# Kernel tuning notes

Hardware: AMD Instinct MI355X
Metric: run time of the kernel (lower is better)

## Reference

```python
import jax, jax.numpy as jnp
import numpy as np

N_NODES = 20000
N_EDGES = 640000
N_GRAPHS = 64
HID = 256
NF = 128
NG = 100   # edge_channels / num_gaussians
NBLK = 6
CUTOFF = 10.0
LOG2 = float(np.log(2.0))


def setup_inputs() -> dict:
    key = jax.random.key(0)
    ks = jax.random.split(key, 24)
    inp = {}
    inp['atom_types'] = jax.random.randint(ks[0], (N_NODES,), 0, 100)
    inp['edge_index'] = jax.random.randint(ks[1], (2, N_EDGES), 0, N_NODES)
    inp['edge_length'] = jax.random.uniform(ks[2], (N_EDGES, 1), jnp.float32) * CUTOFF
    inp['batch_seg'] = jnp.sort(jax.random.randint(ks[3], (N_NODES,), 0, N_GRAPHS))
    s = 0.05
    # embedding table (Embedding(100, hidden); init small so max_norm=10 renorm is inactive)
    inp['atom_emb'] = jax.random.normal(ks[4], (100, HID), jnp.float32) * 0.5
    # per-interaction-block params, stacked on a leading block axis; weights stored [in, out]
    inp['W1s'] = jax.random.normal(ks[5], (NBLK, NG, NF), jnp.float32) * s      # filter MLP lin1
    inp['b1s'] = jnp.zeros((NBLK, NF), jnp.float32)
    inp['W2s'] = jax.random.normal(ks[6], (NBLK, NF, NF), jnp.float32) * s      # filter MLP lin2
    inp['b2s'] = jnp.zeros((NBLK, NF), jnp.float32)
    inp['lin1Ws'] = jax.random.normal(ks[7], (NBLK, HID, NF), jnp.float32) * s  # CFConv.lin1 (no bias)
    inp['lin2Ws'] = jax.random.normal(ks[8], (NBLK, NF, HID), jnp.float32) * s  # CFConv.lin2
    inp['lin2bs'] = jnp.zeros((NBLK, HID), jnp.float32)
    inp['linWs'] = jax.random.normal(ks[9], (NBLK, HID, HID), jnp.float32) * s  # InteractionBlock.lin
    inp['linbs'] = jnp.zeros((NBLK, HID), jnp.float32)
    # final MLP: Linear(256,256) -> act -> Linear(256,256)
    inp['fW1'] = jax.random.normal(ks[10], (HID, HID), jnp.float32) * s
    inp['fb1'] = jnp.zeros((HID,), jnp.float32)
    inp['fW2'] = jax.random.normal(ks[11], (HID, HID), jnp.float32) * s
    inp['fb2'] = jnp.zeros((HID,), jnp.float32)
    return inp


def _ssp(x):
    # ShiftedSoftplus: softplus(x) - log(2)
    return jax.nn.softplus(x) - LOG2


def reference(atom_emb, W1s, b1s, W2s, b2s, lin1Ws, lin2Ws, lin2bs, linWs, linbs,
              fW1, fb1, fW2, fb2, edge_length, atom_types, edge_index, batch_seg):
    n = atom_types.shape[0]
    h = atom_emb[atom_types]                                     # [N, H]
    # Gaussian smearing edge encoder: exp(-0.5/dg^2 * (d - mu_k)^2)
    offsets = jnp.linspace(0.0, CUTOFF, NG)
    coeff = -0.5 / (offsets[1] - offsets[0]) ** 2
    edge_attr = jnp.exp(coeff * (edge_length - offsets[None, :]) ** 2)  # [E, NG]
    # smooth=False cutoff gate
    C = (edge_length <= CUTOFF).astype(h.dtype)                  # [E, 1]
    src, dst = edge_index[0], edge_index[1]
    for i in range(NBLK):
        W = _ssp(edge_attr @ W1s[i] + b1s[i]) @ W2s[i] + b2s[i]  # [E, F]
        W = W * C
        xf = h @ lin1Ws[i]                                       # [N, F]
        msg = xf[src] * W                                        # gather + filter: [E, F]
        agg = jax.ops.segment_sum(msg, dst, num_segments=n)      # scatter-add: [N, F]
        hc = _ssp(agg @ lin2Ws[i] + lin2bs[i])
        hc = hc @ linWs[i] + linbs[i]
        h = h + hc                                               # residual
    pooled = jax.ops.segment_max(h, batch_seg, num_segments=N_GRAPHS)  # global_max_pool
    out = jax.nn.relu(pooled @ fW1 + fb1) @ fW2 + fb2
    return out
```

## Files before the change

kernel.cpp:

```cpp
#include <hip/hip_runtime.h>
#include <math.h>

#define HID 256
#define NF 128
#define NGAUSS 100
#define NBLK 6
#define NGRAPH 64
#define CUTOFF_F 10.0f
#define T_TAB 2048

typedef __attribute__((ext_vector_type(8))) short bf16x8;
typedef __attribute__((ext_vector_type(4))) float f32x4;

__device__ __forceinline__ float ssp(float x) {
    return fmaxf(x, 0.0f) + log1pf(expf(-fabsf(x))) - 0.69314718056f;
}
__device__ __forceinline__ short f2bf(float f) {
    unsigned u = __float_as_uint(f);
    u = u + 0x7fffu + ((u >> 16) & 1u);
    return (short)(u >> 16);
}
__device__ __forceinline__ float bf2f(unsigned s) {
    return __uint_as_float(s << 16);
}
__device__ __forceinline__ unsigned enc_f(float f) {
    unsigned b = __float_as_uint(f);
    return (b & 0x80000000u) ? ~b : (b | 0x80000000u);
}
__device__ __forceinline__ float dec_f(unsigned u) {
    unsigned b = (u & 0x80000000u) ? (u & 0x7FFFFFFFu) : ~u;
    return __uint_as_float(b);
}

__global__ __launch_bounds__(256) void prep_weights(
        const float* __restrict__ W1s,   short* __restrict__ W1Tb,
        const float* __restrict__ W2s,   short* __restrict__ W2Tb,
        const float* __restrict__ lin1Ws, short* __restrict__ lin1T,
        const float* __restrict__ lin2Ws, short* __restrict__ W2T,
        const float* __restrict__ linWs,  short* __restrict__ W3T)
{
    const float* in; short* out; int Ks, Kp, C;
    switch (blockIdx.z) {
        case 0: in = W1s;    out = W1Tb;  Ks = NGAUSS; Kp = NF;  C = NF;  break;
        case 1: in = W2s;    out = W2Tb;  Ks = NF;     Kp = NF;  C = NF;  break;
        case 2: in = lin1Ws; out = lin1T; Ks = HID;    Kp = HID; C = NF;  break;
        case 3: in = lin2Ws; out = W2T;   Ks = NF;     Kp = NF;  C = HID; break;
        default: in = linWs; out = W3T;   Ks = HID;    Kp = HID; C = HID; break;
    }
    int i = blockIdx.y;
    int idx = blockIdx.x * 256 + threadIdx.x;
    if (idx >= Kp * C) return;
    int k = idx / C, c = idx % C;
    out[((size_t)i * C + c) * Kp + k] =
        (k < Ks) ? f2bf(in[((size_t)i * Ks + k) * C + c]) : (short)0;
}

__global__ __launch_bounds__(256) void build_table_mfma(
        const short* __restrict__ W1T, const float* __restrict__ b1s,
        const short* __restrict__ W2T, const float* __restrict__ b2s,
        short* __restrict__ Wtab)
{
    __shared__ short Gs[32 * NF];
    __shared__ short Hs[32 * NF];
    char* gb = (char*)Gs;
    char* hb = (char*)Hs;
    const int i = blockIdx.y;
    const int r0 = blockIdx.x * 32;
    const int wv = threadIdx.x >> 6, lane = threadIdx.x & 63;
    const int lrow = lane & 15, lgrp = lane >> 4;

    const float delta = CUTOFF_F / 99.0f;
    const float coeff = -0.5f / (delta * delta);
    for (int idx = threadIdx.x; idx < 32 * NF; idx += 256) {
        int row = idx >> 7, k = idx & 127;
        float d = (float)(r0 + row) * (CUTOFF_F / (float)(T_TAB - 1));
        float x = d - (float)k * delta;
        float v = (k < NGAUSS) ? expf(coeff * x * x) : 0.0f;
        int byte = idx * 2;
        byte ^= (row & 7) << 4;
        *(short*)(gb + byte) = f2bf(v);
    }
    __syncthreads();

    f32x4 zero = {0.0f, 0.0f, 0.0f, 0.0f};
    f32x4 c1[2][2] = {{zero, zero}, {zero, zero}};
    for (int s = 0; s < 4; ++s) {
        bf16x8 a[2], b[2];
        #pragma unroll
        for (int m = 0; m < 2; ++m) {
            int row = m * 16 + lrow;
            int byte = (row * NF + s * 32 + lgrp * 8) * 2;
            byte ^= (row & 7) << 4;
            a[m] = *(const bf16x8*)(gb + byte);
        }
        #pragma unroll
        for (int n = 0; n < 2; ++n) {
            int col = wv * 32 + n * 16 + lrow;
            b[n] = *(const bf16x8*)(W1T + ((size_t)i * NF + col) * NF + s * 32 + lgrp * 8);
        }
        #pragma unroll
        for (int m = 0; m < 2; ++m)
            #pragma unroll
            for (int n = 0; n < 2; ++n)
                c1[m][n] = __builtin_amdgcn_mfma_f32_16x16x32_bf16(a[m], b[n], c1[m][n], 0, 0, 0);
    }
    #pragma unroll
    for (int m = 0; m < 2; ++m)
        #pragma unroll
        for (int n = 0; n < 2; ++n) {
            int col = wv * 32 + n * 16 + lrow;
            float bb = b1s[i * NF + col];
            #pragma unroll
            for (int j = 0; j < 4; ++j) {
                int row = m * 16 + lgrp * 4 + j;
                int byte = (row * NF + col) * 2;
                byte ^= (row & 7) << 4;
                *(short*)(hb + byte) = f2bf(ssp(c1[m][n][j] + bb));
            }
        }
    __syncthreads();

    f32x4 c2[2][2] = {{zero, zero}, {zero, zero}};
    for (int s = 0; s < 4; ++s) {
        bf16x8 a[2], b[2];
        #pragma unroll
        for (int m = 0; m < 2; ++m) {
            int row = m * 16 + lrow;
            int byte = (row * NF + s * 32 + lgrp * 8) * 2;
            byte ^= (row & 7) << 4;
            a[m] = *(const bf16x8*)(hb + byte);
        }
        #pragma unroll
        for (int n = 0; n < 2; ++n) {
            int col = wv * 32 + n * 16 + lrow;
            b[n] = *(const bf16x8*)(W2T + ((size_t)i * NF + col) * NF + s * 32 + lgrp * 8);
        }
        #pragma unroll
        for (int m = 0; m < 2; ++m)
            #pragma unroll
            for (int n = 0; n < 2; ++n)
                c2[m][n] = __builtin_amdgcn_mfma_f32_16x16x32_bf16(a[m], b[n], c2[m][n], 0, 0, 0);
    }
    #pragma unroll
    for (int m = 0; m < 2; ++m)
        #pragma unroll
        for (int n = 0; n < 2; ++n) {
            int col = wv * 32 + n * 16 + lrow;
            float bb = b2s[i * NF + col];
            #pragma unroll
            for (int j = 0; j < 4; ++j) {
                int t = r0 + m * 16 + lgrp * 4 + j;
                Wtab[((size_t)i * T_TAB + t) * NF + col] = f2bf(c2[m][n][j] + bb);
            }
        }
}

__global__ __launch_bounds__(256) void pack_wtab(
        const short* __restrict__ Wtab, uint2* __restrict__ WtabP)
{
    size_t idx = (size_t)blockIdx.x * 256 + threadIdx.x;
    if (idx >= (size_t)NBLK * (T_TAB + 1) * 64) return;
    int l = (int)(idx & 63);
    int t = (int)((idx >> 6) % (T_TAB + 1));
    int i = (int)(idx / ((size_t)64 * (T_TAB + 1)));
    if (t == T_TAB) { WtabP[idx] = make_uint2(0u, 0u); return; }
    int t1 = (t + 1 < T_TAB) ? t + 1 : t;
    unsigned a = *((const unsigned*)(Wtab + ((size_t)i * T_TAB + t)  * NF) + l);
    unsigned b = *((const unsigned*)(Wtab + ((size_t)i * T_TAB + t1) * NF) + l);
    WtabP[idx] = make_uint2(a, b);
}

__global__ __launch_bounds__(256) void embed_k(
        const float* __restrict__ emb, const int* __restrict__ types,
        float* __restrict__ h, int N)
{
    int gid = blockIdx.x * 256 + threadIdx.x;
    if (gid >= N * HID) return;
    int n = gid >> 8, c = gid & (HID - 1);
    h[gid] = emb[(size_t)types[n] * HID + c];
}

__global__ __launch_bounds__(256) void hist_k(
        const int* __restrict__ dst, int* __restrict__ hist, int E)
{
    int e = blockIdx.x * 256 + threadIdx.x;
    if (e < E) atomicAdd(&hist[dst[e]], 1);
}

__global__ __launch_bounds__(1024) void scan_k(
        const int* __restrict__ in, int* __restrict__ out, int n)
{
    __shared__ int wsum[16];
    __shared__ int carry_s;
    const int tid = threadIdx.x, lane = tid & 63, w = tid >> 6;
    if (tid == 0) carry_s = 0;
    __syncthreads();
    for (int base = 0; base < n; base += 1024) {
        int i = base + tid;
        int v = (i < n) ? in[i] : 0;
        int s = v;
        #pragma unroll
        for (int d = 1; d < 64; d <<= 1) {
            int t = __shfl_up(s, d);
            if (lane >= d) s += t;
        }
        if (lane == 63) wsum[w] = s;
        __syncthreads();
        if (w == 0 && lane < 16) {
            int ws = wsum[lane];
            #pragma unroll
            for (int d = 1; d < 16; d <<= 1) {
                int t = __shfl_up(ws, d);
                if (lane >= d) ws += t;
            }
            wsum[lane] = ws;
        }
        __syncthreads();
        int carry = carry_s;
        if (i < n) out[i] = carry + (w ? wsum[w - 1] : 0) + s - v;
        __syncthreads();
        if (tid == 1023) carry_s = carry + wsum[15];
        __syncthreads();
    }
    if (threadIdx.x == 0) out[n] = carry_s;
}

__global__ __launch_bounds__(256) void scatter_k(
        const int* __restrict__ src, const int* __restrict__ dst,
        const float* __restrict__ elen, const int* __restrict__ off,
        int* __restrict__ cursor, unsigned long long* __restrict__ csr_pk, int E)
{
    int e = blockIdx.x * 256 + threadIdx.x;
    if (e >= E) return;
    int t = dst[e];
    int pos = off[t] + atomicAdd(&cursor[t], 1);
    float d = elen[e];
    float u = d * ((float)(T_TAB - 1) / CUTOFF_F);
    u = fminf(fmaxf(u, 0.0f), (float)(T_TAB - 1) - 1e-3f);
    u = (d <= CUTOFF_F) ? u : (float)T_TAB;
    csr_pk[pos] = ((unsigned long long)__float_as_uint(u) << 32) | (unsigned)src[e];
}

__global__ __launch_bounds__(256) void sort_k(
        const int* __restrict__ off, unsigned long long* __restrict__ csr_pk, int N)
{
    const int node = (blockIdx.x * 256 + threadIdx.x) >> 6;
    const int lane = threadIdx.x & 63;
    if (node >= N) return;
    const int beg = off[node], end = off[node + 1];
    const int deg = end - beg;
    if (deg <= 1) return;
    if (deg <= 128) {
        const unsigned long long PAD = ~0ull;
        unsigned long long v0 = (lane < deg) ? csr_pk[beg + lane] : PAD;
        unsigned long long v1 = (64 + lane < deg) ? csr_pk[beg + 64 + lane] : PAD;
        if (deg > 64) {
            for (int size = 2; size <= 128; size <<= 1)
                for (int stride = size >> 1; stride > 0; stride >>= 1) {
                    if (stride == 64) {
                        unsigned long long lo = v0 < v1 ? v0 : v1;
                        unsigned long long hi = v0 < v1 ? v1 : v0;
                        v0 = lo; v1 = hi;
                    } else {
                        unsigned long long p0 = __shfl_xor(v0, stride);
                        unsigned long long p1 = __shfl_xor(v1, stride);
                        bool up = (lane & stride) != 0;
                        bool d0 = ((lane & size) == 0);
                        bool d1 = (((lane + 64) & size) == 0);
                        v0 = (up ^ d0) ? (v0 < p0 ? v0 : p0) : (v0 > p0 ? v0 : p0);
                        v1 = (up ^ d1) ? (v1 < p1 ? v1 : p1) : (v1 > p1 ? v1 : p1);
                    }
                }
            if (lane < deg) csr_pk[beg + lane] = v0;
            if (64 + lane < deg) csr_pk[beg + 64 + lane] = v1;
        } else {
            for (int size = 2; size <= 64; size <<= 1)
                for (int stride = size >> 1; stride > 0; stride >>= 1) {
                    unsigned long long p0 = __shfl_xor(v0, stride);
                    bool up = (lane & stride) != 0;
                    bool d0 = ((lane & size) == 0);
                    v0 = (up ^ d0) ? (v0 < p0 ? v0 : p0) : (v0 > p0 ? v0 : p0);
                }
            if (lane < deg) csr_pk[beg + lane] = v0;
        }
    } else if (lane == 0) {
        for (int a = beg + 1; a < end; ++a) {
            unsigned long long key = csr_pk[a];
            int b = a - 1;
            while (b >= beg && csr_pk[b] > key) { csr_pk[b + 1] = csr_pk[b]; --b; }
            csr_pk[b + 1] = key;
        }
    }
}


__global__ __launch_bounds__(256) void lin1_k(
        const float* __restrict__ h, const short* __restrict__ lin1T,
        short* __restrict__ xf, int N)
{
    const int wv = threadIdx.x >> 6, lane = threadIdx.x & 63;
    const int lrow = lane & 15, lgrp = lane >> 4;
    const int wrow = wv >> 1, wcol = wv & 1;
    const int r0 = blockIdx.x * 64 + wrow * 32;

    f32x4 zero = {0.0f, 0.0f, 0.0f, 0.0f};
    f32x4 c[2][4] = {{zero, zero, zero, zero}, {zero, zero, zero, zero}};

    for (int s = 0; s < 8; ++s) {
        bf16x8 a[2], b[4];
        #pragma unroll
        for (int m = 0; m < 2; ++m) {
            int row = r0 + m * 16 + lrow;
            if (row >= N) row = N - 1;
            const float* hp = h + (size_t)row * HID + s * 32 + lgrp * 8;
            float4 p0 = *(const float4*)hp;
            float4 p1 = *(const float4*)(hp + 4);
            bf16x8 t;
            t[0] = f2bf(p0.x); t[1] = f2bf(p0.y); t[2] = f2bf(p0.z); t[3] = f2bf(p0.w);
            t[4] = f2bf(p1.x); t[5] = f2bf(p1.y); t[6] = f2bf(p1.z); t[7] = f2bf(p1.w);
            a[m] = t;
        }
        #pragma unroll
        for (int n = 0; n < 4; ++n) {
            int col = wcol * 64 + n * 16 + lrow;
            b[n] = *(const bf16x8*)(lin1T + (size_t)col * HID + s * 32 + lgrp * 8);
        }
        #pragma unroll
        for (int m = 0; m < 2; ++m)
            #pragma unroll
            for (int n = 0; n < 4; ++n)
                c[m][n] = __builtin_amdgcn_mfma_f32_16x16x32_bf16(a[m], b[n], c[m][n], 0, 0, 0);
    }
    #pragma unroll
    for (int m = 0; m < 2; ++m)
        #pragma unroll
        for (int n = 0; n < 4; ++n) {
            int col = wcol * 64 + n * 16 + lrow;
            #pragma unroll
            for (int j = 0; j < 4; ++j) {
                int row = r0 + m * 16 + lgrp * 4 + j;
                if (row < N) xf[(size_t)row * NF + col] = f2bf(c[m][n][j]);
            }
        }
}

__global__ __launch_bounds__(256) void agg_k(
        const short* __restrict__ xf, const uint2* __restrict__ wt,
        const int* __restrict__ off, const unsigned long long* __restrict__ csr_pk,
        short* __restrict__ agg, int N)
{
    const int node = (blockIdx.x * 256 + threadIdx.x) >> 6;
    const int lane = threadIdx.x & 63;
    if (node >= N) return;
    const int beg = __builtin_amdgcn_readfirstlane(off[node]);
    const int end = __builtin_amdgcn_readfirstlane(off[node + 1]);
    float a0 = 0.0f, a1 = 0.0f;

    int k = beg;
    for (; k + 16 <= end; k += 16) {
        unsigned long long pk[16];
        #pragma unroll
        for (int q = 0; q < 16; ++q) pk[q] = csr_pk[k + q];
        uint2 wp[16];
        unsigned xv[16];
        float fr[16];
        #pragma unroll
        for (int q = 0; q < 16; ++q) {
            int s = (int)(unsigned)pk[q];
            float uf = __uint_as_float((unsigned)(pk[q] >> 32));
            int i0 = (int)uf;
            fr[q] = uf - (float)i0;
            wp[q] = wt[(size_t)i0 * 64 + lane];
            xv[q] = *(const unsigned*)(xf + (size_t)s * NF + 2 * lane);
        }
        #pragma unroll
        for (int q = 0; q < 16; ++q) {
            float w0a = bf2f(wp[q].x & 0xffffu), w0b = bf2f(wp[q].x >> 16);
            float w1a = bf2f(wp[q].y & 0xffffu), w1b = bf2f(wp[q].y >> 16);
            float xa  = bf2f(xv[q] & 0xffffu), xb  = bf2f(xv[q] >> 16);
            a0 = fmaf(xa, fmaf(fr[q], w1a - w0a, w0a), a0);
            a1 = fmaf(xb, fmaf(fr[q], w1b - w0b, w0b), a1);
        }
    }
    for (; k + 8 <= end; k += 8) {
        unsigned long long pk[8];
        #pragma unroll
        for (int q = 0; q < 8; ++q) pk[q] = csr_pk[k + q];
        uint2 wp[8];
        unsigned xv[8];
        float fr[8];
        #pragma unroll
        for (int q = 0; q < 8; ++q) {
            int s = (int)(unsigned)pk[q];
            float uf = __uint_as_float((unsigned)(pk[q] >> 32));
            int i0 = (int)uf;
            fr[q] = uf - (float)i0;
            wp[q] = wt[(size_t)i0 * 64 + lane];
            xv[q] = *(const unsigned*)(xf + (size_t)s * NF + 2 * lane);
        }
        #pragma unroll
        for (int q = 0; q < 8; ++q) {
            float w0a = bf2f(wp[q].x & 0xffffu), w0b = bf2f(wp[q].x >> 16);
            float w1a = bf2f(wp[q].y & 0xffffu), w1b = bf2f(wp[q].y >> 16);
            float xa  = bf2f(xv[q] & 0xffffu), xb  = bf2f(xv[q] >> 16);
            a0 = fmaf(xa, fmaf(fr[q], w1a - w0a, w0a), a0);
            a1 = fmaf(xb, fmaf(fr[q], w1b - w0b, w0b), a1);
        }
    }
    if (k < end) {
        const int rem = end - k;
        unsigned long long pk[8];
        #pragma unroll
        for (int q = 0; q < 8; ++q) {
            int kk = k + q < end ? k + q : end - 1;
            pk[q] = csr_pk[kk];
        }
        uint2 wp[8];
        unsigned xv[8];
        float fr[8];
        #pragma unroll
        for (int q = 0; q < 8; ++q) {
            int s = (int)(unsigned)pk[q];
            float uf = __uint_as_float((unsigned)(pk[q] >> 32));
            int i0 = (int)uf;
            fr[q] = uf - (float)i0;
            wp[q] = wt[(size_t)i0 * 64 + lane];
            xv[q] = *(const unsigned*)(xf + (size_t)s * NF + 2 * lane);
        }
        #pragma unroll
        for (int q = 0; q < 8; ++q) {
            float g = (q < rem) ? 1.0f : 0.0f;
            float w0a = bf2f(wp[q].x & 0xffffu), w0b = bf2f(wp[q].x >> 16);
            float w1a = bf2f(wp[q].y & 0xffffu), w1b = bf2f(wp[q].y >> 16);
            float xa  = bf2f(xv[q] & 0xffffu), xb  = bf2f(xv[q] >> 16);
            a0 = fmaf(xa * g, fmaf(fr[q], w1a - w0a, w0a), a0);
            a1 = fmaf(xb * g, fmaf(fr[q], w1b - w0b, w0b), a1);
        }
    }
    unsigned pack = (unsigned)(unsigned short)f2bf(a0)
                  | ((unsigned)(unsigned short)f2bf(a1) << 16);
    *(unsigned*)(agg + (size_t)node * NF + 2 * lane) = pack;
}

__global__ __launch_bounds__(512) void update_k(
        const short* __restrict__ aggb, const short* __restrict__ W2T,
        const float* __restrict__ b2, const short* __restrict__ W3T,
        const float* __restrict__ b3, float* __restrict__ h,
        const short* __restrict__ lin1Tn, short* __restrict__ xf_out, int N)
{
    __shared__ short tmp[32 * HID];
    __shared__ float ftmp[32][HID + 4];
    char* tb = (char*)tmp;
    const int wv = threadIdx.x >> 6, lane = threadIdx.x & 63;
    const int lrow = lane & 15, lgrp = lane >> 4;
    const int r0 = blockIdx.x * 32;

    f32x4 zero = {0.0f, 0.0f, 0.0f, 0.0f};
    f32x4 c1[2][2] = {{zero, zero}, {zero, zero}};

    for (int s = 0; s < 4; ++s) {
        bf16x8 a[2], b[2];
        #pragma unroll
        for (int m = 0; m < 2; ++m) {
            int row = r0 + m * 16 + lrow;
            if (row >= N) row = N - 1;
            a[m] = *(const bf16x8*)(aggb + (size_t)row * NF + s * 32 + lgrp * 8);
        }
        #pragma unroll
        for (int n = 0; n < 2; ++n) {
            int col = wv * 32 + n * 16 + lrow;
            b[n] = *(const bf16x8*)(W2T + (size_t)col * NF + s * 32 + lgrp * 8);
        }
        #pragma unroll
        for (int m = 0; m < 2; ++m)
            #pragma unroll
            for (int n = 0; n < 2; ++n)
                c1[m][n] = __builtin_amdgcn_mfma_f32_16x16x32_bf16(a[m], b[n], c1[m][n], 0, 0, 0);
    }
    #pragma unroll
    for (int m = 0; m < 2; ++m)
        #pragma unroll
        for (int n = 0; n < 2; ++n) {
            int col = wv * 32 + n * 16 + lrow;
            float bb = b2[col];
            #pragma unroll
            for (int j = 0; j < 4; ++j) {
                int row = m * 16 + lgrp * 4 + j;
                int byte = (row * HID + col) * 2;
                byte ^= (row & 7) << 4;
                *(short*)(tb + byte) = f2bf(ssp(c1[m][n][j] + bb));
            }
        }
    __syncthreads();

    f32x4 c2[2][2] = {{zero, zero}, {zero, zero}};
    for (int s = 0; s < 8; ++s) {
        bf16x8 a[2], b[2];
        #pragma unroll
        for (int m = 0; m < 2; ++m) {
            int row = m * 16 + lrow;
            int byte = (row * HID + s * 32 + lgrp * 8) * 2;
            byte ^= (row & 7) << 4;
            a[m] = *(const bf16x8*)(tb + byte);
        }
        #pragma unroll
        for (int n = 0; n < 2; ++n) {
            int col = wv * 32 + n * 16 + lrow;
            b[n] = *(const bf16x8*)(W3T + (size_t)col * HID + s * 32 + lgrp * 8);
        }
        #pragma unroll
        for (int m = 0; m < 2; ++m)
            #pragma unroll
            for (int n = 0; n < 2; ++n)
                c2[m][n] = __builtin_amdgcn_mfma_f32_16x16x32_bf16(a[m], b[n], c2[m][n], 0, 0, 0);
    }

    #pragma unroll
    for (int m = 0; m < 2; ++m)
        #pragma unroll
        for (int n = 0; n < 2; ++n) {
            int col = wv * 32 + n * 16 + lrow;
            float bb = b3[col];
            #pragma unroll
            for (int j = 0; j < 4; ++j)
                ftmp[m * 16 + lgrp * 4 + j][col] = c2[m][n][j] + bb;
        }
    __syncthreads();

    {
        const int r  = threadIdx.x >> 4;
        const int c0 = (threadIdx.x & 15) * 4;
        const int row = r0 + r;
        const bool valid = row < N;
        float* hp = h + (size_t)row * HID;
        #pragma unroll
        for (int k = 0; k < 4; ++k) {
            int col = c0 + k * 64;
            float4 hv = valid ? *(const float4*)(hp + col)
                              : make_float4(0.f, 0.f, 0.f, 0.f);
            float4 f = *(const float4*)&ftmp[r][col];
            hv.x += f.x; hv.y += f.y; hv.z += f.z; hv.w += f.w;
            if (valid) *(float4*)(hp + col) = hv;
            short4 s4;
            s4.x = f2bf(hv.x); s4.y = f2bf(hv.y); s4.z = f2bf(hv.z); s4.w = f2bf(hv.w);
            int byte = (r * HID + col) * 2;
            byte ^= (r & 7) << 4;
            *(short4*)(tb + byte) = s4;
        }
    }
    if (xf_out == nullptr) return;
    __syncthreads();

    f32x4 c3[2] = {zero, zero};
    for (int s = 0; s < 8; ++s) {
        bf16x8 a[2], b;
        #pragma unroll
        for (int m = 0; m < 2; ++m) {
            int row = m * 16 + lrow;
            int byte = (row * HID + s * 32 + lgrp * 8) * 2;
            byte ^= (row & 7) << 4;
            a[m] = *(const bf16x8*)(tb + byte);
        }
        {
            int col = wv * 16 + lrow;
            b = *(const bf16x8*)(lin1Tn + (size_t)col * HID + s * 32 + lgrp * 8);
        }
        #pragma unroll
        for (int m = 0; m < 2; ++m)
            c3[m] = __builtin_amdgcn_mfma_f32_16x16x32_bf16(a[m], b, c3[m], 0, 0, 0);
    }
    #pragma unroll
    for (int m = 0; m < 2; ++m) {
        int col = wv * 16 + lrow;
        #pragma unroll
        for (int j = 0; j < 4; ++j) {
            int row = r0 + m * 16 + lgrp * 4 + j;
            if (row < N) xf_out[(size_t)row * NF + col] = f2bf(c3[m][j]);
        }
    }
}

__global__ __launch_bounds__(256) void pool_init(unsigned* __restrict__ pe)
{
    int i = blockIdx.x * 256 + threadIdx.x;
    if (i < NGRAPH * HID) pe[i] = enc_f(-INFINITY);
}

__global__ __launch_bounds__(256) void pool_max2(
        const float* __restrict__ h, const int* __restrict__ seg,
        unsigned* __restrict__ pe, int N)
{
    const int c = threadIdx.x;
    const int base = blockIdx.x * 64;
    if (base >= N) return;
    int cur = seg[base];
    float m = -INFINITY;
    for (int r = 0; r < 64; ++r) {
        int row = base + r;
        if (row >= N) break;
        int s = seg[row];
        if (s != cur) {
            atomicMax(&pe[(size_t)cur * HID + c], enc_f(m));
            m = -INFINITY;
            cur = s;
        }
        m = fmaxf(m, h[(size_t)row * HID + c]);
    }
    atomicMax(&pe[(size_t)cur * HID + c], enc_f(m));
}

__global__ __launch_bounds__(1024) void final_mlp(
        const unsigned* __restrict__ pe,
        const float* __restrict__ fW1, const float* __restrict__ fb1,
        const float* __restrict__ fW2, const float* __restrict__ fb2,
        float* __restrict__ out)
{
    __shared__ float p[HID];
    __shared__ float part[4][HID];
    __shared__ float p2[HID];
    const int g = blockIdx.x;
    const int c = threadIdx.x & 255;
    const int kq = threadIdx.x >> 8;
    if (threadIdx.x < HID) p[threadIdx.x] = dec_f(pe[(size_t)g * HID + threadIdx.x]);
    __syncthreads();
    float a = 0.0f;
    #pragma unroll 8
    for (int k = kq * 64; k < kq * 64 + 64; ++k)
        a = fmaf(p[k], fW1[(size_t)k * HID + c], a);
    part[kq][c] = a;
    __syncthreads();
    if (kq == 0) {
        float s = part[0][c] + part[1][c] + part[2][c] + part[3][c] + fb1[c];
        p2[c] = fmaxf(s, 0.0f);
    }
    __syncthreads();
    float o = 0.0f;
    #pragma unroll 8
    for (int k = kq * 64; k < kq * 64 + 64; ++k)
        o = fmaf(p2[k], fW2[(size_t)k * HID + c], o);
    part[kq][c] = o;
    __syncthreads();
    if (kq == 0)
        out[(size_t)g * HID + c] = part[0][c] + part[1][c] + part[2][c] + part[3][c] + fb2[c];
}

extern "C" void kernel_launch(void* const* d_in, const int* in_sizes, int n_in,
                              void* d_out, int out_size, void* d_ws, size_t ws_size,
                              hipStream_t stream)
{
    const int*   atom_types = (const int*)  d_in[0];
    const int*   edge_index = (const int*)  d_in[1];
    const float* edge_len   = (const float*)d_in[2];
    const int*   batch_seg  = (const int*)  d_in[3];
    const float* atom_emb   = (const float*)d_in[4];
    const float* W1s    = (const float*)d_in[5];
    const float* b1s    = (const float*)d_in[6];
    const float* W2s    = (const float*)d_in[7];
    const float* b2s    = (const float*)d_in[8];
    const float* lin1Ws = (const float*)d_in[9];
    const float* lin2Ws = (const float*)d_in[10];
    const float* lin2bs = (const float*)d_in[11];
    const float* linWs  = (const float*)d_in[12];
    const float* linbs  = (const float*)d_in[13];
    const float* fW1    = (const float*)d_in[14];
    const float* fb1    = (const float*)d_in[15];
    const float* fW2    = (const float*)d_in[16];
    const float* fb2    = (const float*)d_in[17];

    const int N = in_sizes[0];
    const int E = in_sizes[1] / 2;
    const int* src = edge_index;
    const int* dst = edge_index + E;

    char* ws = (char*)d_ws;
    float* h     = (float*)ws;  ws += (size_t)N * HID * sizeof(float);
    short* xf    = (short*)ws;  ws += (size_t)N * NF * sizeof(short);
    short* aggb  = (short*)ws;  ws += (size_t)N * NF * sizeof(short);
    short* Wtab  = (short*)ws;  ws += (size_t)NBLK * T_TAB * NF * sizeof(short);
    uint2* WtabP = (uint2*)ws;  ws += (size_t)NBLK * (T_TAB + 1) * 64 * sizeof(uint2);
    short* lin1T = (short*)ws;  ws += (size_t)NBLK * NF * HID * sizeof(short);
    short* W2T   = (short*)ws;  ws += (size_t)NBLK * HID * NF * sizeof(short);
    short* W3T   = (short*)ws;  ws += (size_t)NBLK * HID * HID * sizeof(short);
    short* W1Tb  = (short*)ws;  ws += (size_t)NBLK * NF * NF * sizeof(short);
    short* W2Tb  = (short*)ws;  ws += (size_t)NBLK * NF * NF * sizeof(short);
    unsigned* pooled = (unsigned*)ws;   ws += (size_t)NGRAPH * HID * sizeof(unsigned);
    unsigned long long* csr_pk = (unsigned long long*)ws; ws += (size_t)E * sizeof(unsigned long long);
    int* hist    = (int*)ws;  ws += (size_t)N * sizeof(int);
    int* off     = (int*)ws;  ws += (size_t)(N + 1) * sizeof(int);
    int* cursor  = (int*)ws;

    hipMemsetAsync(hist, 0, (size_t)N * sizeof(int), stream);
    hipMemsetAsync(cursor, 0, (size_t)N * sizeof(int), stream);
    hist_k<<<(E + 255) / 256, 256, 0, stream>>>(dst, hist, E);
    scan_k<<<1, 1024, 0, stream>>>(hist, off, N);
    scatter_k<<<(E + 255) / 256, 256, 0, stream>>>(src, dst, edge_len, off,
                                                   cursor, csr_pk, E);
    sort_k<<<(N * 64 + 255) / 256, 256, 0, stream>>>(off, csr_pk, N);

    prep_weights<<<dim3((HID * HID + 255) / 256, NBLK, 5), 256, 0, stream>>>(
        W1s, W1Tb, W2s, W2Tb, lin1Ws, lin1T, lin2Ws, W2T, linWs, W3T);

    build_table_mfma<<<dim3(T_TAB / 32, NBLK), 256, 0, stream>>>(W1Tb, b1s, W2Tb, b2s, Wtab);
    pack_wtab<<<(int)(((size_t)NBLK * (T_TAB + 1) * 64 + 255) / 256), 256, 0, stream>>>(Wtab, WtabP);
    embed_k<<<(N * HID + 255) / 256, 256, 0, stream>>>(atom_emb, atom_types, h, N);
    lin1_k<<<(N + 63) / 64, 256, 0, stream>>>(h, lin1T, xf, N);

    for (int i = 0; i < NBLK; ++i) {
        agg_k<<<(N * 64 + 255) / 256, 256, 0, stream>>>(
            xf, WtabP + (size_t)i * (T_TAB + 1) * 64, off, csr_pk, aggb, N);
        update_k<<<(N + 31) / 32, 512, 0, stream>>>(
            aggb, W2T + (size_t)i * HID * NF, lin2bs + (size_t)i * HID,
            W3T + (size_t)i * HID * HID, linbs + (size_t)i * HID, h,
            lin1T + (size_t)(i + 1) * NF * HID,
            (i < NBLK - 1) ? xf : nullptr, N);
    }

    pool_init<<<(NGRAPH * HID + 255) / 256, 256, 0, stream>>>(pooled);
    pool_max2<<<(N + 63) / 64, 256, 0, stream>>>(h, batch_seg, pooled, N);
    final_mlp<<<NGRAPH, 1024, 0, stream>>>(pooled, fW1, fb1, fW2, fb2, (float*)d_out);
}
```

Measured before the change: 620.8 us.

## Fuse max pooling into final MLP and drop 16-edge unroll in aggregation

Replaces pool_init, the atomic segment-max kernel and the final MLP with one kernel per graph. Each block binary-searches the sorted batch_seg for its node range, takes the max over its rows, then runs both MLP layers with 256 threads. This removes two launches and the atomics, but each of the 64 blocks now reads its whole segment serially. Separately, the agg_k gather loop loses its 16-edge unrolled stage and falls back to the 8-edge loop, which lowers register pressure but leaves fewer loads in flight per wave.

```diff
diff --git a/kernel.cpp b/kernel.cpp
--- a/kernel.cpp
+++ b/kernel.cpp
@@ -22,14 +22,6 @@
 }
 __device__ __forceinline__ float bf2f(unsigned s) {
     return __uint_as_float(s << 16);
-}
-__device__ __forceinline__ unsigned enc_f(float f) {
-    unsigned b = __float_as_uint(f);
-    return (b & 0x80000000u) ? ~b : (b | 0x80000000u);
-}
-__device__ __forceinline__ float dec_f(unsigned u) {
-    unsigned b = (u & 0x80000000u) ? (u & 0x7FFFFFFFu) : ~u;
-    return __uint_as_float(b);
 }
 
 __global__ __launch_bounds__(256) void prep_weights(
@@ -357,31 +349,6 @@
     float a0 = 0.0f, a1 = 0.0f;
 
     int k = beg;
-    for (; k + 16 <= end; k += 16) {
-        unsigned long long pk[16];
-        #pragma unroll
-        for (int q = 0; q < 16; ++q) pk[q] = csr_pk[k + q];
-        uint2 wp[16];
-        unsigned xv[16];
-        float fr[16];
-        #pragma unroll
-        for (int q = 0; q < 16; ++q) {
-            int s = (int)(unsigned)pk[q];
-            float uf = __uint_as_float((unsigned)(pk[q] >> 32));
-            int i0 = (int)uf;
-            fr[q] = uf - (float)i0;
-            wp[q] = wt[(size_t)i0 * 64 + lane];
-            xv[q] = *(const unsigned*)(xf + (size_t)s * NF + 2 * lane);
-        }
-        #pragma unroll
-        for (int q = 0; q < 16; ++q) {
-            float w0a = bf2f(wp[q].x & 0xffffu), w0b = bf2f(wp[q].x >> 16);
-            float w1a = bf2f(wp[q].y & 0xffffu), w1b = bf2f(wp[q].y >> 16);
-            float xa  = bf2f(xv[q] & 0xffffu), xb  = bf2f(xv[q] >> 16);
-            a0 = fmaf(xa, fmaf(fr[q], w1a - w0a, w0a), a0);
-            a1 = fmaf(xb, fmaf(fr[q], w1b - w0b, w0b), a1);
-        }
-    }
     for (; k + 8 <= end; k += 8) {
         unsigned long long pk[8];
         #pragma unroll
@@ -580,68 +547,46 @@
     }
 }
 
-__global__ __launch_bounds__(256) void pool_init(unsigned* __restrict__ pe)
-{
-    int i = blockIdx.x * 256 + threadIdx.x;
-    if (i < NGRAPH * HID) pe[i] = enc_f(-INFINITY);
-}
-
-__global__ __launch_bounds__(256) void pool_max2(
+__global__ __launch_bounds__(256) void pool_mlp(
         const float* __restrict__ h, const int* __restrict__ seg,
-        unsigned* __restrict__ pe, int N)
-{
-    const int c = threadIdx.x;
-    const int base = blockIdx.x * 64;
-    if (base >= N) return;
-    int cur = seg[base];
-    float m = -INFINITY;
-    for (int r = 0; r < 64; ++r) {
-        int row = base + r;
-        if (row >= N) break;
-        int s = seg[row];
-        if (s != cur) {
-            atomicMax(&pe[(size_t)cur * HID + c], enc_f(m));
-            m = -INFINITY;
-            cur = s;
-        }
-        m = fmaxf(m, h[(size_t)row * HID + c]);
-    }
-    atomicMax(&pe[(size_t)cur * HID + c], enc_f(m));
-}
-
-__global__ __launch_bounds__(1024) void final_mlp(
-        const unsigned* __restrict__ pe,
         const float* __restrict__ fW1, const float* __restrict__ fb1,
         const float* __restrict__ fW2, const float* __restrict__ fb2,
-        float* __restrict__ out)
+        float* __restrict__ out, int N)
 {
     __shared__ float p[HID];
-    __shared__ float part[4][HID];
-    __shared__ float p2[HID];
-    const int g = blockIdx.x;
-    const int c = threadIdx.x & 255;
-    const int kq = threadIdx.x >> 8;
-    if (threadIdx.x < HID) p[threadIdx.x] = dec_f(pe[(size_t)g * HID + threadIdx.x]);
-    __syncthreads();
-    float a = 0.0f;
+    __shared__ float tbuf[HID];
+    const int g = blockIdx.x, c = threadIdx.x;
+
+    int lo, hi;
+    {
+        int a = 0, b = N;
+        while (a < b) { int m = (a + b) >> 1; if (seg[m] < g) a = m + 1; else b = m; }
+        lo = a;
+        b = N;
+        while (a < b) { int m = (a + b) >> 1; if (seg[m] < g + 1) a = m + 1; else b = m; }
+        hi = a;
+    }
+    float m0 = -INFINITY, m1 = -INFINITY, m2 = -INFINITY, m3 = -INFINITY;
+    int r = lo;
+    for (; r + 4 <= hi; r += 4) {
+        m0 = fmaxf(m0, h[(size_t)(r    ) * HID + c]);
+        m1 = fmaxf(m1, h[(size_t)(r + 1) * HID + c]);
+        m2 = fmaxf(m2, h[(size_t)(r + 2) * HID + c]);
+        m3 = fmaxf(m3, h[(size_t)(r + 3) * HID + c]);
+    }
+    for (; r < hi; ++r) m0 = fmaxf(m0, h[(size_t)r * HID + c]);
+    p[c] = fmaxf(fmaxf(m0, m1), fmaxf(m2, m3));
+    __syncthreads();
+
+    float a1 = fb1[c];
     #pragma unroll 8
-    for (int k = kq * 64; k < kq * 64 + 64; ++k)
-        a = fmaf(p[k], fW1[(size_t)k * HID + c], a);
-    part[kq][c] = a;
-    __syncthreads();
-    if (kq == 0) {
-        float s = part[0][c] + part[1][c] + part[2][c] + part[3][c] + fb1[c];
-        p2[c] = fmaxf(s, 0.0f);
-    }
-    __syncthreads();
-    float o = 0.0f;
+    for (int k = 0; k < HID; ++k) a1 = fmaf(p[k], fW1[(size_t)k * HID + c], a1);
+    tbuf[c] = fmaxf(a1, 0.0f);
+    __syncthreads();
+    float o = fb2[c];
     #pragma unroll 8
-    for (int k = kq * 64; k < kq * 64 + 64; ++k)
-        o = fmaf(p2[k], fW2[(size_t)k * HID + c], o);
-    part[kq][c] = o;
-    __syncthreads();
-    if (kq == 0)
-        out[(size_t)g * HID + c] = part[0][c] + part[1][c] + part[2][c] + part[3][c] + fb2[c];
+    for (int k = 0; k < HID; ++k) o = fmaf(tbuf[k], fW2[(size_t)k * HID + c], o);
+    out[(size_t)g * HID + c] = o;
 }
 
 extern "C" void kernel_launch(void* const* d_in, const int* in_sizes, int n_in,
@@ -683,7 +628,6 @@
     short* W3T   = (short*)ws;  ws += (size_t)NBLK * HID * HID * sizeof(short);
     short* W1Tb  = (short*)ws;  ws += (size_t)NBLK * NF * NF * sizeof(short);
     short* W2Tb  = (short*)ws;  ws += (size_t)NBLK * NF * NF * sizeof(short);
-    unsigned* pooled = (unsigned*)ws;   ws += (size_t)NGRAPH * HID * sizeof(unsigned);
     unsigned long long* csr_pk = (unsigned long long*)ws; ws += (size_t)E * sizeof(unsigned long long);
     int* hist    = (int*)ws;  ws += (size_t)N * sizeof(int);
     int* off     = (int*)ws;  ws += (size_t)(N + 1) * sizeof(int);
@@ -715,7 +659,6 @@
             (i < NBLK - 1) ? xf : nullptr, N);
     }
 
-    pool_init<<<(NGRAPH * HID + 255) / 256, 256, 0, stream>>>(pooled);
-    pool_max2<<<(N + 63) / 64, 256, 0, stream>>>(h, batch_seg, pooled, N);
-    final_mlp<<<NGRAPH, 1024, 0, stream>>>(pooled, fW1, fb1, fW2, fb2, (float*)d_out);
-}
+    pool_mlp<<<NGRAPH, 256, 0, stream>>>(h, batch_seg, fW1, fb1, fW2, fb2,
+                                         (float*)d_out, N);
+}
```

Result: no change. 610.1 us (-1.7%).
